# Performance work log

Hardware: AMD Instinct MI355X
Metric: run time of the kernel (lower is better)

The kernel has to match this reference:

```python
import jax, jax.numpy as jnp
import numpy as np


def setup_inputs() -> dict:
    key = jax.random.key(0)
    k1, _ = jax.random.split(key)
    N, H, CH, T = 4, 8, 64, 2048
    qkv = jax.random.normal(k1, (N, H * 3 * CH, T), dtype=jnp.float32)
    rescale = jnp.ones((1,), dtype=jnp.float32)
    return {"qkv": qkv, "rescale": rescale, "n_heads": H}


def reference(qkv, rescale, n_heads):
    bs, width, length = qkv.shape
    ch = width // (3 * n_heads)
    # [N, H*3*C, T] -> [N*H, 3*C, T] -> three [N*H, C, T]
    qkv_h = qkv.reshape(bs * n_heads, 3 * ch, length)
    q, k, v = qkv_h[:, :ch], qkv_h[:, ch:2 * ch], qkv_h[:, 2 * ch:]
    scale = 1.0 / jnp.sqrt(jnp.sqrt(jnp.float32(ch)))
    # scores: [B*H, T, S]
    weight = jnp.einsum('bct,bcs->bts', q * scale, k * scale)
    weight = jax.nn.softmax(weight.astype(jnp.float32) * rescale[0], axis=-1).astype(qkv.dtype)
    a = jnp.einsum('bts,bcs->bct', weight, v)  # [B*H, C, T]
    return a.reshape(bs, n_heads * ch, length)
```

## Files before the change

### kernel.cpp

```cpp
#include <hip/hip_runtime.h>

typedef _Float16 half8 __attribute__((ext_vector_type(8)));
typedef _Float16 half4 __attribute__((ext_vector_type(4)));
typedef float    floatx4 __attribute__((ext_vector_type(4)));

#define T_LEN 2048
#define CH 64
#define BH 32
#define QTILE 128
#define LDP 72
#define FRAG_BH 131072

__global__ __launch_bounds__(256, 2)
void prep_kernel(const float* __restrict__ qkv, _Float16* __restrict__ ws)
{
    __shared__ _Float16 Qs[64][LDP];
    __shared__ _Float16 Ks[64][LDP];
    __shared__ _Float16 Vs[64][LDP];

    const int tid  = threadIdx.x;
    const int bh   = blockIdx.y;
    const int tile = blockIdx.x;
    const int x0   = tile * 64;

    const float* qp = qkv + (size_t)(bh >> 3) * (1536 * T_LEN)
                          + (size_t)(bh & 7) * (192 * T_LEN);
    const float* kp = qp + 64 * T_LEN;
    const float* vp = qp + 128 * T_LEN;

    {
        const int a4 = (tid & 15) * 4;
        const int c4 = (tid >> 4) * 4;
        float4 rq[4], rk[4];
#pragma unroll
        for (int i = 0; i < 4; ++i) {
            rq[i] = *(const float4*)(qp + (size_t)(c4 + i) * T_LEN + x0 + a4);
            rk[i] = *(const float4*)(kp + (size_t)(c4 + i) * T_LEN + x0 + a4);
        }
#pragma unroll
        for (int j = 0; j < 4; ++j) {
            half4 hq, hk;
#pragma unroll
            for (int i = 0; i < 4; ++i) {
                hq[i] = (_Float16)((&rq[i].x)[j]);
                hk[i] = (_Float16)((&rk[i].x)[j]);
            }
            *(half4*)&Qs[a4 + j][c4] = hq;
            *(half4*)&Ks[a4 + j][c4] = hk;
        }
        const int s4 = (tid & 15) * 4;
        const int cv = tid >> 4;
#pragma unroll
        for (int i = 0; i < 4; ++i) {
            const int c = cv + 16 * i;
            float4 r = *(const float4*)(vp + (size_t)c * T_LEN + x0 + s4);
            half4 h; h[0]=(_Float16)r.x; h[1]=(_Float16)r.y; h[2]=(_Float16)r.z; h[3]=(_Float16)r.w;
            *(half4*)&Vs[c][s4] = h;
        }
    }
    __syncthreads();

    const int lane = tid & 63, wave = tid >> 6;
    const int l15 = lane & 15, quad = lane >> 4;
    _Float16* qf = ws;
    _Float16* kf = ws + (size_t)BH * FRAG_BH;
    _Float16* vf = ws + (size_t)2 * BH * FRAG_BH;

#pragma unroll
    for (int ks = 0; ks < 2; ++ks) {
        half8 hq = *(const half8*)&Qs[wave * 16 + l15][ks * 32 + quad * 8];
        half8 hk = *(const half8*)&Ks[wave * 16 + l15][ks * 32 + quad * 8];
        half8 hv = *(const half8*)&Vs[wave * 16 + l15][ks * 32 + quad * 8];
        const size_t gqk = (((size_t)bh * 128 + tile * 4 + wave) * 2 + ks) * 512 + lane * 8;
        *(half8*)(qf + gqk) = hq;
        *(half8*)(kf + gqk) = hk;
        *(half8*)(vf + (((size_t)bh * 32 + tile) * 8 + wave * 2 + ks) * 512 + lane * 8) = hv;
    }
}

__global__ __launch_bounds__(256, 2)
void attn_kernel(const _Float16* __restrict__ ws, const float* __restrict__ rescale,
                 float* __restrict__ out)
{
    __shared__ _Float16 Pt[4][32][LDP];

    const int tid  = threadIdx.x;
    const int wave = tid >> 6;
    const int lane = tid & 63;
    const int l15  = lane & 15;
    const int quad = lane >> 4;

    const int bh = blockIdx.y;
    const int t0 = blockIdx.x * QTILE;

    const _Float16* qf = ws;
    const _Float16* kf = ws + (size_t)BH * FRAG_BH;
    const _Float16* vf = ws + (size_t)2 * BH * FRAG_BH;
    float* op = out + (size_t)bh * (CH * T_LEN);

    const float fscale = 0.125f * rescale[0];

    half8 bq[2][2];
#pragma unroll
    for (int tb = 0; tb < 2; ++tb)
#pragma unroll
        for (int ks = 0; ks < 2; ++ks)
            bq[tb][ks] = *(const half8*)(qf +
                (((size_t)bh * 128 + (t0 >> 4) + wave * 2 + tb) * 2 + ks) * 512 + lane * 8);

    const floatx4 fzero = {0.f, 0.f, 0.f, 0.f};
    floatx4 oacc[2][4];
#pragma unroll
    for (int tb = 0; tb < 2; ++tb)
#pragma unroll
        for (int ct = 0; ct < 4; ++ct) oacc[tb][ct] = fzero;
    float lsum[2] = {0.f, 0.f};

    const _Float16* kfp = kf + (size_t)bh * FRAG_BH + lane * 8;
    const _Float16* vfp = vf + (size_t)bh * FRAG_BH + lane * 8;

    for (int st = 0; st < 32; ++st) {
        half8 ak[4][2];
#pragma unroll
        for (int mt = 0; mt < 4; ++mt)
#pragma unroll
            for (int ks = 0; ks < 2; ++ks)
                ak[mt][ks] = *(const half8*)(kfp + (size_t)(mt * 2 + ks) * 512);
        half8 bv[4][2];
#pragma unroll
        for (int ct = 0; ct < 4; ++ct)
#pragma unroll
            for (int ks = 0; ks < 2; ++ks)
                bv[ct][ks] = *(const half8*)(vfp + (size_t)(ct * 2 + ks) * 512);
        kfp += 4096;
        vfp += 4096;

        floatx4 sacc[4][2];
#pragma unroll
        for (int mt = 0; mt < 4; ++mt)
#pragma unroll
            for (int tb = 0; tb < 2; ++tb) sacc[mt][tb] = fzero;
#pragma unroll
        for (int mt = 0; mt < 4; ++mt)
#pragma unroll
            for (int tb = 0; tb < 2; ++tb)
#pragma unroll
                for (int ks = 0; ks < 2; ++ks)
                    sacc[mt][tb] = __builtin_amdgcn_mfma_f32_16x16x32_f16(
                        ak[mt][ks], bq[tb][ks], sacc[mt][tb], 0, 0, 0);

#pragma unroll
        for (int mt = 0; mt < 4; ++mt)
#pragma unroll
            for (int tb = 0; tb < 2; ++tb) {
                half4 ph;
#pragma unroll
                for (int r = 0; r < 4; ++r) {
                    float p = __expf(sacc[mt][tb][r] * fscale);
                    lsum[tb] += p;
                    ph[r] = (_Float16)p;
                }
                *(half4*)&Pt[wave][tb * 16 + l15][mt * 16 + quad * 4] = ph;
            }
        asm volatile("s_waitcnt lgkmcnt(0)" ::: "memory");

        half8 ap[2][2];
#pragma unroll
        for (int tb = 0; tb < 2; ++tb)
#pragma unroll
            for (int ks = 0; ks < 2; ++ks)
                ap[tb][ks] = *(const half8*)&Pt[wave][tb * 16 + l15][ks * 32 + quad * 8];

#pragma unroll
        for (int tb = 0; tb < 2; ++tb)
#pragma unroll
            for (int ct = 0; ct < 4; ++ct)
#pragma unroll
                for (int ks = 0; ks < 2; ++ks)
                    oacc[tb][ct] = __builtin_amdgcn_mfma_f32_16x16x32_f16(
                        ap[tb][ks], bv[ct][ks], oacc[tb][ct], 0, 0, 0);
    }

#pragma unroll
    for (int tb = 0; tb < 2; ++tb) {
        lsum[tb] += __shfl_xor(lsum[tb], 16);
        lsum[tb] += __shfl_xor(lsum[tb], 32);
        lsum[tb] = 1.0f / lsum[tb];
    }
    float linv[2][4];
#pragma unroll
    for (int tb = 0; tb < 2; ++tb)
#pragma unroll
        for (int r = 0; r < 4; ++r)
            linv[tb][r] = __shfl(lsum[tb], quad * 4 + r);

#pragma unroll
    for (int tb = 0; tb < 2; ++tb)
#pragma unroll
        for (int ct = 0; ct < 4; ++ct) {
            const int c = ct * 16 + l15;
            const int t = t0 + wave * 32 + tb * 16 + quad * 4;
            float4 o;
#pragma unroll
            for (int r = 0; r < 4; ++r)
                (&o.x)[r] = oacc[tb][ct][r] * linv[tb][r];
            *(float4*)(op + (size_t)c * T_LEN + t) = o;
        }
}

extern "C" void kernel_launch(void* const* d_in, const int* in_sizes, int n_in,
                              void* d_out, int out_size, void* d_ws, size_t ws_size,
                              hipStream_t stream) {
    const float* qkv     = (const float*)d_in[0];
    const float* rescale = (const float*)d_in[1];
    float* out = (float*)d_out;
    _Float16* ws = (_Float16*)d_ws;

    prep_kernel<<<dim3(32, BH), dim3(256), 0, stream>>>(qkv, ws);
    attn_kernel<<<dim3(T_LEN / QTILE, BH), dim3(256), 0, stream>>>(ws, rescale, out);
}
```

Baseline: 152.1 us.

## Halve query tile, fold softmax scale into Q, compute row sums via MFMA

The attention kernel now gives each wave 16 query rows instead of 32, doubling the grid and raising the launch-bounds occupancy target to 4 blocks per CU. The scale and log2(e) factor are folded into Q during the prep pass, so the inner loop uses a raw exp2 with no multiply. Softmax row sums are accumulated by an extra MFMA against a ones vector, which replaces the per-element adds and the final shuffles. In exchange, every loaded K/V fragment is reused across half as many queries, which doubles K/V traffic per query. The sums are also taken from fp16-rounded probabilities, and the exp is still not max-subtracted.

```diff
diff --git a/kernel.cpp b/kernel.cpp
--- a/kernel.cpp
+++ b/kernel.cpp
@@ -7,12 +7,13 @@
 #define T_LEN 2048
 #define CH 64
 #define BH 32
-#define QTILE 128
+#define QTILE 64
 #define LDP 72
 #define FRAG_BH 131072
 
 __global__ __launch_bounds__(256, 2)
-void prep_kernel(const float* __restrict__ qkv, _Float16* __restrict__ ws)
+void prep_kernel(const float* __restrict__ qkv, const float* __restrict__ rescale,
+                 _Float16* __restrict__ ws)
 {
     __shared__ _Float16 Qs[64][LDP];
     __shared__ _Float16 Ks[64][LDP];
@@ -22,6 +23,8 @@
     const int bh   = blockIdx.y;
     const int tile = blockIdx.x;
     const int x0   = tile * 64;
+
+    const float qscale = 0.125f * 1.4426950408889634f * rescale[0];
 
     const float* qp = qkv + (size_t)(bh >> 3) * (1536 * T_LEN)
                           + (size_t)(bh & 7) * (192 * T_LEN);
@@ -42,7 +45,7 @@
             half4 hq, hk;
 #pragma unroll
             for (int i = 0; i < 4; ++i) {
-                hq[i] = (_Float16)((&rq[i].x)[j]);
+                hq[i] = (_Float16)((&rq[i].x)[j] * qscale);
                 hk[i] = (_Float16)((&rk[i].x)[j]);
             }
             *(half4*)&Qs[a4 + j][c4] = hq;
@@ -78,11 +81,10 @@
     }
 }
 
-__global__ __launch_bounds__(256, 2)
-void attn_kernel(const _Float16* __restrict__ ws, const float* __restrict__ rescale,
-                 float* __restrict__ out)
+__global__ __launch_bounds__(256, 4)
+void attn_kernel(const _Float16* __restrict__ ws, float* __restrict__ out)
 {
-    __shared__ _Float16 Pt[4][32][LDP];
+    __shared__ _Float16 Pt[4][16][LDP];
 
     const int tid  = threadIdx.x;
     const int wave = tid >> 6;
@@ -98,114 +100,88 @@
     const _Float16* vf = ws + (size_t)2 * BH * FRAG_BH;
     float* op = out + (size_t)bh * (CH * T_LEN);
 
-    const float fscale = 0.125f * rescale[0];
-
-    half8 bq[2][2];
+    half8 bq[2];
 #pragma unroll
-    for (int tb = 0; tb < 2; ++tb)
-#pragma unroll
-        for (int ks = 0; ks < 2; ++ks)
-            bq[tb][ks] = *(const half8*)(qf +
-                (((size_t)bh * 128 + (t0 >> 4) + wave * 2 + tb) * 2 + ks) * 512 + lane * 8);
+    for (int ks = 0; ks < 2; ++ks)
+        bq[ks] = *(const half8*)(qf +
+            (((size_t)bh * 128 + blockIdx.x * 4 + wave) * 2 + ks) * 512 + lane * 8);
 
     const floatx4 fzero = {0.f, 0.f, 0.f, 0.f};
-    floatx4 oacc[2][4];
+    floatx4 oacc[4];
 #pragma unroll
-    for (int tb = 0; tb < 2; ++tb)
+    for (int ct = 0; ct < 4; ++ct) oacc[ct] = fzero;
+    floatx4 lacc = fzero;
+
+    half8 bones;
 #pragma unroll
-        for (int ct = 0; ct < 4; ++ct) oacc[tb][ct] = fzero;
-    float lsum[2] = {0.f, 0.f};
+    for (int i = 0; i < 8; ++i) bones[i] = (_Float16)1.0f;
 
     const _Float16* kfp = kf + (size_t)bh * FRAG_BH + lane * 8;
     const _Float16* vfp = vf + (size_t)bh * FRAG_BH + lane * 8;
 
     for (int st = 0; st < 32; ++st) {
-        half8 ak[4][2];
+        half8 ak[4][2], bv[4][2];
+#pragma unroll
+        for (int mt = 0; mt < 4; ++mt)
+#pragma unroll
+            for (int ks = 0; ks < 2; ++ks) {
+                ak[mt][ks] = *(const half8*)(kfp + (size_t)(mt * 2 + ks) * 512);
+                bv[mt][ks] = *(const half8*)(vfp + (size_t)(mt * 2 + ks) * 512);
+            }
+        kfp += 4096;
+        vfp += 4096;
+
+        floatx4 sacc[4];
+#pragma unroll
+        for (int mt = 0; mt < 4; ++mt) sacc[mt] = fzero;
 #pragma unroll
         for (int mt = 0; mt < 4; ++mt)
 #pragma unroll
             for (int ks = 0; ks < 2; ++ks)
-                ak[mt][ks] = *(const half8*)(kfp + (size_t)(mt * 2 + ks) * 512);
-        half8 bv[4][2];
+                sacc[mt] = __builtin_amdgcn_mfma_f32_16x16x32_f16(
+                    ak[mt][ks], bq[ks], sacc[mt], 0, 0, 0);
+
+#pragma unroll
+        for (int mt = 0; mt < 4; ++mt) {
+            half4 ph;
+#pragma unroll
+            for (int r = 0; r < 4; ++r)
+                ph[r] = (_Float16)__builtin_amdgcn_exp2f(sacc[mt][r]);
+            *(half4*)&Pt[wave][l15][mt * 16 + quad * 4] = ph;
+        }
+        asm volatile("s_waitcnt lgkmcnt(0)" ::: "memory");
+
+        half8 ap[2];
+#pragma unroll
+        for (int ks = 0; ks < 2; ++ks)
+            ap[ks] = *(const half8*)&Pt[wave][l15][ks * 32 + quad * 8];
+
+#pragma unroll
+        for (int ks = 0; ks < 2; ++ks)
+            lacc = __builtin_amdgcn_mfma_f32_16x16x32_f16(ap[ks], bones, lacc, 0, 0, 0);
+
 #pragma unroll
         for (int ct = 0; ct < 4; ++ct)
 #pragma unroll
             for (int ks = 0; ks < 2; ++ks)
-                bv[ct][ks] = *(const half8*)(vfp + (size_t)(ct * 2 + ks) * 512);
-        kfp += 4096;
-        vfp += 4096;
+                oacc[ct] = __builtin_amdgcn_mfma_f32_16x16x32_f16(
+                    ap[ks], bv[ct][ks], oacc[ct], 0, 0, 0);
+    }
 
-        floatx4 sacc[4][2];
+    float linv[4];
 #pragma unroll
-        for (int mt = 0; mt < 4; ++mt)
-#pragma unroll
-            for (int tb = 0; tb < 2; ++tb) sacc[mt][tb] = fzero;
-#pragma unroll
-        for (int mt = 0; mt < 4; ++mt)
-#pragma unroll
-            for (int tb = 0; tb < 2; ++tb)
-#pragma unroll
-                for (int ks = 0; ks < 2; ++ks)
-                    sacc[mt][tb] = __builtin_amdgcn_mfma_f32_16x16x32_f16(
-                        ak[mt][ks], bq[tb][ks], sacc[mt][tb], 0, 0, 0);
+    for (int r = 0; r < 4; ++r) linv[r] = 1.0f / lacc[r];
 
 #pragma unroll
-        for (int mt = 0; mt < 4; ++mt)
-#pragma unroll
-            for (int tb = 0; tb < 2; ++tb) {
-                half4 ph;
-#pragma unroll
-                for (int r = 0; r < 4; ++r) {
-                    float p = __expf(sacc[mt][tb][r] * fscale);
-                    lsum[tb] += p;
-                    ph[r] = (_Float16)p;
-                }
-                *(half4*)&Pt[wave][tb * 16 + l15][mt * 16 + quad * 4] = ph;
-            }
-        asm volatile("s_waitcnt lgkmcnt(0)" ::: "memory");
-
-        half8 ap[2][2];
-#pragma unroll
-        for (int tb = 0; tb < 2; ++tb)
-#pragma unroll
-            for (int ks = 0; ks < 2; ++ks)
-                ap[tb][ks] = *(const half8*)&Pt[wave][tb * 16 + l15][ks * 32 + quad * 8];
-
-#pragma unroll
-        for (int tb = 0; tb < 2; ++tb)
-#pragma unroll
-            for (int ct = 0; ct < 4; ++ct)
-#pragma unroll
-                for (int ks = 0; ks < 2; ++ks)
-                    oacc[tb][ct] = __builtin_amdgcn_mfma_f32_16x16x32_f16(
-                        ap[tb][ks], bv[ct][ks], oacc[tb][ct], 0, 0, 0);
-    }
-
-#pragma unroll
-    for (int tb = 0; tb < 2; ++tb) {
-        lsum[tb] += __shfl_xor(lsum[tb], 16);
-        lsum[tb] += __shfl_xor(lsum[tb], 32);
-        lsum[tb] = 1.0f / lsum[tb];
-    }
-    float linv[2][4];
-#pragma unroll
-    for (int tb = 0; tb < 2; ++tb)
+    for (int ct = 0; ct < 4; ++ct) {
+        const int c = ct * 16 + l15;
+        const int t = t0 + wave * 16 + quad * 4;
+        float4 o;
 #pragma unroll
         for (int r = 0; r < 4; ++r)
-            linv[tb][r] = __shfl(lsum[tb], quad * 4 + r);
-
-#pragma unroll
-    for (int tb = 0; tb < 2; ++tb)
-#pragma unroll
-        for (int ct = 0; ct < 4; ++ct) {
-            const int c = ct * 16 + l15;
-            const int t = t0 + wave * 32 + tb * 16 + quad * 4;
-            float4 o;
-#pragma unroll
-            for (int r = 0; r < 4; ++r)
-                (&o.x)[r] = oacc[tb][ct][r] * linv[tb][r];
-            *(float4*)(op + (size_t)c * T_LEN + t) = o;
-        }
+            (&o.x)[r] = oacc[ct][r] * linv[r];
+        *(float4*)(op + (size_t)c * T_LEN + t) = o;
+    }
 }
 
 extern "C" void kernel_launch(void* const* d_in, const int* in_sizes, int n_in,
@@ -216,6 +192,6 @@
     float* out = (float*)d_out;
     _Float16* ws = (_Float16*)d_ws;
 
-    prep_kernel<<<dim3(32, BH), dim3(256), 0, stream>>>(qkv, ws);
-    attn_kernel<<<dim3(T_LEN / QTILE, BH), dim3(256), 0, stream>>>(ws, rescale, out);
+    prep_kernel<<<dim3(32, BH), dim3(256), 0, stream>>>(qkv, rescale, ws);
+    attn_kernel<<<dim3(T_LEN / QTILE, BH), dim3(256), 0, stream>>>(ws, out);
 }
```

Measured after the change: 159.4 us. 4.8% more time.

## Double-buffer K/V tiles in LDS via async loads, fold scale into Q, row sums via MFMA

Applied to the files above, without the earlier changes.

Replaces the per-wave direct global loads of K and V fragments with block-shared LDS tiles. These are filled by global_load_lds async copies into two buffers, so the next tile loads while the current one is computed. The softmax scale and log2(e) are folded into Q during the prep kernel, so the inner loop uses a bare exp2. The row sums are accumulated with an extra MFMA against a ones vector instead of scalar adds and shuffles. The cost is a block-wide barrier every iteration and more LDS use. The kernel still skips max subtraction, and Q is now scaled before the fp16 conversion, which shifts rounding slightly.

```diff
diff --git a/kernel.cpp b/kernel.cpp
--- a/kernel.cpp
+++ b/kernel.cpp
@@ -1,4 +1,5 @@
 #include <hip/hip_runtime.h>
+#include <stdint.h>
 
 typedef _Float16 half8 __attribute__((ext_vector_type(8)));
 typedef _Float16 half4 __attribute__((ext_vector_type(4)));
@@ -9,10 +10,18 @@
 #define BH 32
 #define QTILE 128
 #define LDP 72
+#define PTP 72
 #define FRAG_BH 131072
 
+__device__ __forceinline__ void load16_lds(const _Float16* g, const _Float16* l) {
+    __builtin_amdgcn_global_load_lds(
+        (const __attribute__((address_space(1))) uint32_t*)(uintptr_t)g,
+        (__attribute__((address_space(3))) uint32_t*)(uintptr_t)l, 16, 0, 0);
+}
+
 __global__ __launch_bounds__(256, 2)
-void prep_kernel(const float* __restrict__ qkv, _Float16* __restrict__ ws)
+void prep_kernel(const float* __restrict__ qkv, const float* __restrict__ rescale,
+                 _Float16* __restrict__ ws)
 {
     __shared__ _Float16 Qs[64][LDP];
     __shared__ _Float16 Ks[64][LDP];
@@ -23,6 +32,8 @@
     const int tile = blockIdx.x;
     const int x0   = tile * 64;
 
+    const float qscale = 0.125f * 1.4426950408889634f * rescale[0];
+
     const float* qp = qkv + (size_t)(bh >> 3) * (1536 * T_LEN)
                           + (size_t)(bh & 7) * (192 * T_LEN);
     const float* kp = qp + 64 * T_LEN;
@@ -42,7 +53,7 @@
             half4 hq, hk;
 #pragma unroll
             for (int i = 0; i < 4; ++i) {
-                hq[i] = (_Float16)((&rq[i].x)[j]);
+                hq[i] = (_Float16)((&rq[i].x)[j] * qscale);
                 hk[i] = (_Float16)((&rk[i].x)[j]);
             }
             *(half4*)&Qs[a4 + j][c4] = hq;
@@ -79,10 +90,11 @@
 }
 
 __global__ __launch_bounds__(256, 2)
-void attn_kernel(const _Float16* __restrict__ ws, const float* __restrict__ rescale,
-                 float* __restrict__ out)
+void attn_kernel(const _Float16* __restrict__ ws, float* __restrict__ out)
 {
-    __shared__ _Float16 Pt[4][32][LDP];
+    __shared__ _Float16 KL[2][4096];
+    __shared__ _Float16 VL[2][4096];
+    __shared__ _Float16 Pt[4][32][PTP];
 
     const int tid  = threadIdx.x;
     const int wave = tid >> 6;
@@ -98,7 +110,8 @@
     const _Float16* vf = ws + (size_t)2 * BH * FRAG_BH;
     float* op = out + (size_t)bh * (CH * T_LEN);
 
-    const float fscale = 0.125f * rescale[0];
+    const _Float16* ktile = kf + (size_t)bh * FRAG_BH;
+    const _Float16* vtile = vf + (size_t)bh * FRAG_BH;
 
     half8 bq[2][2];
 #pragma unroll
@@ -106,7 +119,7 @@
 #pragma unroll
         for (int ks = 0; ks < 2; ++ks)
             bq[tb][ks] = *(const half8*)(qf +
-                (((size_t)bh * 128 + (t0 >> 4) + wave * 2 + tb) * 2 + ks) * 512 + lane * 8);
+                (((size_t)bh * 128 + blockIdx.x * 8 + wave * 2 + tb) * 2 + ks) * 512 + lane * 8);
 
     const floatx4 fzero = {0.f, 0.f, 0.f, 0.f};
     floatx4 oacc[2][4];
@@ -114,26 +127,41 @@
     for (int tb = 0; tb < 2; ++tb)
 #pragma unroll
         for (int ct = 0; ct < 4; ++ct) oacc[tb][ct] = fzero;
-    float lsum[2] = {0.f, 0.f};
-
-    const _Float16* kfp = kf + (size_t)bh * FRAG_BH + lane * 8;
-    const _Float16* vfp = vf + (size_t)bh * FRAG_BH + lane * 8;
-
+    floatx4 lacc[2] = {fzero, fzero};
+
+    half8 bones;
+#pragma unroll
+    for (int i = 0; i < 8; ++i) bones[i] = (_Float16)1.0f;
+
+#pragma unroll
+    for (int c = 0; c < 2; ++c) {
+        load16_lds(ktile + wave * 1024 + c * 512 + lane * 8, &KL[0][wave * 1024 + c * 512]);
+        load16_lds(vtile + wave * 1024 + c * 512 + lane * 8, &VL[0][wave * 1024 + c * 512]);
+    }
+    __syncthreads();
+
+#pragma unroll 1
     for (int st = 0; st < 32; ++st) {
-        half8 ak[4][2];
-#pragma unroll
-        for (int mt = 0; mt < 4; ++mt)
-#pragma unroll
-            for (int ks = 0; ks < 2; ++ks)
-                ak[mt][ks] = *(const half8*)(kfp + (size_t)(mt * 2 + ks) * 512);
-        half8 bv[4][2];
-#pragma unroll
-        for (int ct = 0; ct < 4; ++ct)
-#pragma unroll
-            for (int ks = 0; ks < 2; ++ks)
-                bv[ct][ks] = *(const half8*)(vfp + (size_t)(ct * 2 + ks) * 512);
-        kfp += 4096;
-        vfp += 4096;
+        const int buf = st & 1;
+
+        if (st < 31) {
+            const _Float16* kg = ktile + (size_t)(st + 1) * 4096;
+            const _Float16* vg = vtile + (size_t)(st + 1) * 4096;
+#pragma unroll
+            for (int c = 0; c < 2; ++c) {
+                load16_lds(kg + wave * 1024 + c * 512 + lane * 8, &KL[buf ^ 1][wave * 1024 + c * 512]);
+                load16_lds(vg + wave * 1024 + c * 512 + lane * 8, &VL[buf ^ 1][wave * 1024 + c * 512]);
+            }
+        }
+
+        half8 ak[4][2], bv[4][2];
+#pragma unroll
+        for (int mt = 0; mt < 4; ++mt)
+#pragma unroll
+            for (int ks = 0; ks < 2; ++ks) {
+                ak[mt][ks] = *(const half8*)&KL[buf][(mt * 2 + ks) * 512 + lane * 8];
+                bv[mt][ks] = *(const half8*)&VL[buf][(mt * 2 + ks) * 512 + lane * 8];
+            }
 
         floatx4 sacc[4][2];
 #pragma unroll
@@ -155,14 +183,10 @@
             for (int tb = 0; tb < 2; ++tb) {
                 half4 ph;
 #pragma unroll
-                for (int r = 0; r < 4; ++r) {
-                    float p = __expf(sacc[mt][tb][r] * fscale);
-                    lsum[tb] += p;
-                    ph[r] = (_Float16)p;
-                }
+                for (int r = 0; r < 4; ++r)
+                    ph[r] = (_Float16)__builtin_amdgcn_exp2f(sacc[mt][tb][r]);
                 *(half4*)&Pt[wave][tb * 16 + l15][mt * 16 + quad * 4] = ph;
             }
-        asm volatile("s_waitcnt lgkmcnt(0)" ::: "memory");
 
         half8 ap[2][2];
 #pragma unroll
@@ -171,6 +195,11 @@
             for (int ks = 0; ks < 2; ++ks)
                 ap[tb][ks] = *(const half8*)&Pt[wave][tb * 16 + l15][ks * 32 + quad * 8];
 
+#pragma unroll
+        for (int tb = 0; tb < 2; ++tb)
+#pragma unroll
+            for (int ks = 0; ks < 2; ++ks)
+                lacc[tb] = __builtin_amdgcn_mfma_f32_16x16x32_f16(ap[tb][ks], bones, lacc[tb], 0, 0, 0);
 #pragma unroll
         for (int tb = 0; tb < 2; ++tb)
 #pragma unroll
@@ -179,23 +208,15 @@
                 for (int ks = 0; ks < 2; ++ks)
                     oacc[tb][ct] = __builtin_amdgcn_mfma_f32_16x16x32_f16(
                         ap[tb][ks], bv[ct][ks], oacc[tb][ct], 0, 0, 0);
+
+        __syncthreads();
     }
 
 #pragma unroll
     for (int tb = 0; tb < 2; ++tb) {
-        lsum[tb] += __shfl_xor(lsum[tb], 16);
-        lsum[tb] += __shfl_xor(lsum[tb], 32);
-        lsum[tb] = 1.0f / lsum[tb];
-    }
-    float linv[2][4];
-#pragma unroll
-    for (int tb = 0; tb < 2; ++tb)
-#pragma unroll
-        for (int r = 0; r < 4; ++r)
-            linv[tb][r] = __shfl(lsum[tb], quad * 4 + r);
-
-#pragma unroll
-    for (int tb = 0; tb < 2; ++tb)
+        float linv[4];
+#pragma unroll
+        for (int r = 0; r < 4; ++r) linv[r] = 1.0f / lacc[tb][r];
 #pragma unroll
         for (int ct = 0; ct < 4; ++ct) {
             const int c = ct * 16 + l15;
@@ -203,9 +224,10 @@
             float4 o;
 #pragma unroll
             for (int r = 0; r < 4; ++r)
-                (&o.x)[r] = oacc[tb][ct][r] * linv[tb][r];
+                (&o.x)[r] = oacc[tb][ct][r] * linv[r];
             *(float4*)(op + (size_t)c * T_LEN + t) = o;
         }
+    }
 }
 
 extern "C" void kernel_launch(void* const* d_in, const int* in_sizes, int n_in,
@@ -216,6 +238,6 @@
     float* out = (float*)d_out;
     _Float16* ws = (_Float16*)d_ws;
 
-    prep_kernel<<<dim3(32, BH), dim3(256), 0, stream>>>(qkv, ws);
-    attn_kernel<<<dim3(T_LEN / QTILE, BH), dim3(256), 0, stream>>>(ws, rescale, out);
-}
+    prep_kernel<<<dim3(32, BH), dim3(256), 0, stream>>>(qkv, rescale, ws);
+    attn_kernel<<<dim3(T_LEN / QTILE, BH), dim3(256), 0, stream>>>(ws, out);
+}
```

Measured after the change: 137.2 us. 9.8% less time.
